# Optimization experiments

Measured on AMD Instinct MI355X. Metric: run time of the kernel, lower is better.

The kernel has to match this reference:

```python
import jax, jax.numpy as jnp
import numpy as np

N = 50000          # nodes
E = 800000         # directed edges (before self-loops)
IN_C = 512
HID = 256
HEADS = 8
HEAD_C = HID // HEADS
OUT_C = 64
NEG_SLOPE = 0.2    # PyG GATConv default LeakyReLU slope
EPS = 1e-16        # PyG softmax denominator epsilon


def _gat_layer(h, src, dst, a_src, a_dst):
    """One GATConv propagate step (eval mode, no attention dropout).
    h: [N, H, C] transformed node features; src/dst: [Etot] edge endpoints.
    Returns aggregated [N, H, C]."""
    # per-node attention logits: [N, H]
    alpha_src = jnp.einsum('nhc,hc->nh', h, a_src)
    alpha_dst = jnp.einsum('nhc,hc->nh', h, a_dst)
    e = alpha_src[src] + alpha_dst[dst]                      # [Etot, H]
    e = jnp.where(e > 0, e, NEG_SLOPE * e)                   # LeakyReLU
    # segment softmax over incoming edges of each dst node
    e_max = jax.ops.segment_max(e, dst, num_segments=N)      # [N, H]
    e_exp = jnp.exp(e - e_max[dst])                          # [Etot, H]
    denom = jax.ops.segment_sum(e_exp, dst, num_segments=N)  # [N, H]
    alpha = e_exp / (denom[dst] + EPS)                       # [Etot, H]
    msg = alpha[:, :, None] * h[src]                         # [Etot, H, C]
    return jax.ops.segment_sum(msg, dst, num_segments=N)     # [N, H, C]


def setup_inputs() -> dict:
    key = jax.random.key(0)
    ks = jax.random.split(key, 10)
    s1 = 1.0 / np.sqrt(IN_C)
    s2 = 1.0 / np.sqrt(HID)
    return {
        'x': jax.random.normal(ks[0], (N, IN_C), jnp.float32),
        'edge_index': jax.random.randint(ks[1], (2, E), 0, N, dtype=jnp.int64),
        'W1': jax.random.normal(ks[2], (IN_C, HID), jnp.float32) * s1,
        'a_src1': jax.random.normal(ks[3], (HEADS, HEAD_C), jnp.float32) * 0.1,
        'a_dst1': jax.random.normal(ks[4], (HEADS, HEAD_C), jnp.float32) * 0.1,
        'b1': jnp.zeros((HID,), jnp.float32),
        'W2': jax.random.normal(ks[5], (HID, OUT_C), jnp.float32) * s2,
        'a_src2': jax.random.normal(ks[6], (1, OUT_C), jnp.float32) * 0.1,
        'a_dst2': jax.random.normal(ks[7], (1, OUT_C), jnp.float32) * 0.1,
        'b2': jnp.zeros((OUT_C,), jnp.float32),
    }


def reference(x, edge_index, W1, a_src1, a_dst1, b1, W2, a_src2, a_dst2, b2):
    # PyG GATConv: add self-loops (default add_self_loops=True)
    loops = jnp.arange(N, dtype=edge_index.dtype)
    src = jnp.concatenate([edge_index[0], loops])
    dst = jnp.concatenate([edge_index[1], loops])

    # conv1: heads=8, concat=True
    h1 = (x @ W1).reshape(N, HEADS, HEAD_C)
    h1 = _gat_layer(h1, src, dst, a_src1, a_dst1).reshape(N, HID) + b1
    h1 = jax.nn.elu(h1)

    # conv2: heads=1, concat=False (mean over 1 head == identity)
    h2 = (h1 @ W2).reshape(N, 1, OUT_C)
    out = _gat_layer(h2, src, dst, a_src2, a_dst2).mean(axis=1) + b2
    return out
```

## Files before the change

### kernel.cpp

```cpp
#include <hip/hip_runtime.h>

#define N_NODES 50000
#define M_PAD   50048
#define NBLK    196
#define E_EDGES 800000
#define E_TOT   (E_EDGES + N_NODES)
#define IN_C 512
#define HID 256
#define HEADS 8
#define OUT_C 64

typedef unsigned int uint;
typedef unsigned short ushort_t;
typedef __bf16 bf16x8 __attribute__((ext_vector_type(8)));
typedef float f32x4 __attribute__((ext_vector_type(4)));
typedef float f32x2 __attribute__((ext_vector_type(2)));

__device__ __forceinline__ float lrelu(float x) { return x > 0.f ? x : 0.2f * x; }

__device__ __forceinline__ unsigned short f2bf(float f) {
  __bf16 b = (__bf16)f;
  return __builtin_bit_cast(unsigned short, b);
}
__device__ __forceinline__ float bflo(uint u) { return __uint_as_float(u << 16); }
__device__ __forceinline__ float bfhi(uint u) { return __uint_as_float(u & 0xFFFF0000u); }
__device__ __forceinline__ f32x2 unp2(uint u) {
  f32x2 r; r.x = bflo(u); r.y = bfhi(u); return r;
}

__global__ void k_count(const int* __restrict__ ei, int* __restrict__ counts) {
  int e = blockIdx.x * blockDim.x + threadIdx.x;
  if (e >= E_TOT) return;
  int d = (e < E_EDGES) ? ei[E_EDGES + e] : (e - E_EDGES);
  atomicAdd(&counts[d], 1);
}

__global__ void k_bsum(const int* __restrict__ counts, int* __restrict__ bsum) {
  int i = blockIdx.x * 256 + threadIdx.x;
  int v = (i < N_NODES) ? counts[i] : 0;
  __shared__ int ws[4];
  int lane = threadIdx.x & 63, wid = threadIdx.x >> 6;
  #pragma unroll
  for (int off = 32; off; off >>= 1) v += __shfl_xor(v, off);
  if (lane == 0) ws[wid] = v;
  __syncthreads();
  if (threadIdx.x == 0) bsum[blockIdx.x] = ws[0] + ws[1] + ws[2] + ws[3];
}

__global__ void k_bscan(const int* __restrict__ bsum, int* __restrict__ boff) {
  int tid = threadIdx.x;
  int v = (tid < NBLK) ? bsum[tid] : 0;
  int lane = tid & 63, wid = tid >> 6;
  int x = v;
  #pragma unroll
  for (int off = 1; off < 64; off <<= 1) {
    int t = __shfl_up(x, off);
    if (lane >= off) x += t;
  }
  __shared__ int ws[4];
  if (lane == 63) ws[wid] = x;
  __syncthreads();
  int woff = 0;
  for (int w = 0; w < wid; w++) woff += ws[w];
  if (tid < NBLK) boff[tid] = x + woff - v;
}

__global__ void k_local(const int* __restrict__ counts, const int* __restrict__ boff,
                        int* __restrict__ indptr, int* __restrict__ wptr) {
  int b = blockIdx.x;
  int i = b * 256 + threadIdx.x;
  int v = (i < N_NODES) ? counts[i] : 0;
  int lane = threadIdx.x & 63, wid = threadIdx.x >> 6;
  int x = v;
  #pragma unroll
  for (int off = 1; off < 64; off <<= 1) {
    int t = __shfl_up(x, off);
    if (lane >= off) x += t;
  }
  __shared__ int ws[4];
  if (lane == 63) ws[wid] = x;
  __syncthreads();
  int woff = boff[b];
  for (int w = 0; w < wid; w++) woff += ws[w];
  int excl = woff + x - v;
  if (i < N_NODES) { indptr[i] = excl; wptr[i] = excl; }
  if (b == 0 && threadIdx.x == 0) indptr[N_NODES] = E_TOT;
}

__global__ void k_scatter(const int* __restrict__ ei, int* __restrict__ wptr,
                          int* __restrict__ csr_src) {
  int e = blockIdx.x * blockDim.x + threadIdx.x;
  if (e >= E_TOT) return;
  int s, d;
  if (e < E_EDGES) { s = ei[e]; d = ei[E_EDGES + e]; }
  else { s = d = e - E_EDGES; }
  int pos = atomicAdd(&wptr[d], 1);
  csr_src[pos] = s;
}

__global__ void k_convw(const float* __restrict__ W1, const float* __restrict__ W2,
                        ushort_t* __restrict__ w1t, ushort_t* __restrict__ w2t) {
  int t = blockIdx.x * blockDim.x + threadIdx.x;
  if (t < HID * IN_C) {
    int n = t >> 9, k = t & 511;
    w1t[t] = f2bf(W1[(size_t)k * HID + n]);
  } else if (t < HID * IN_C + OUT_C * HID) {
    int u = t - HID * IN_C;
    int n = u >> 8, k = u & 255;
    w2t[u] = f2bf(W2[(size_t)k * OUT_C + n]);
  }
}

__global__ __launch_bounds__(512) void k_mm1(const float* __restrict__ A,
                                             const ushort_t* __restrict__ Bt,
                                             const float* __restrict__ asrc1,
                                             const float* __restrict__ adst1,
                                             ushort_t* __restrict__ Cb,
                                             float* __restrict__ as1,
                                             float* __restrict__ ad1) {
  __shared__ ushort_t sA[128][40];
  __shared__ ushort_t sB[256][40];
  int tid = threadIdx.x;
  int wid = tid >> 6, lane = tid & 63;
  int wm = wid >> 2, wn = wid & 3;
  int lr = lane & 15, kg = lane >> 4;
  int row0 = blockIdx.x * 128;
  f32x4 acc[4][4] = {};

  for (int k0 = 0; k0 < IN_C; k0 += 32) {
    {
      int r = tid >> 2, cs = (tid & 3) * 8;
      int gr = row0 + r;
      unsigned short v[8];
      if (gr < N_NODES) {
        const float* src = A + (size_t)gr * IN_C + k0 + cs;
        float4 f0 = *reinterpret_cast<const float4*>(src);
        float4 f1 = *reinterpret_cast<const float4*>(src + 4);
        v[0] = f2bf(f0.x); v[1] = f2bf(f0.y); v[2] = f2bf(f0.z); v[3] = f2bf(f0.w);
        v[4] = f2bf(f1.x); v[5] = f2bf(f1.y); v[6] = f2bf(f1.z); v[7] = f2bf(f1.w);
      } else {
        #pragma unroll
        for (int i = 0; i < 8; i++) v[i] = 0;
      }
      uint4 pk;
      pk.x = v[0] | ((uint)v[1] << 16); pk.y = v[2] | ((uint)v[3] << 16);
      pk.z = v[4] | ((uint)v[5] << 16); pk.w = v[6] | ((uint)v[7] << 16);
      *reinterpret_cast<uint4*>(&sA[r][cs]) = pk;
    }
    {
      int n = tid >> 1, ks = (tid & 1) * 16;
      const ushort_t* src = Bt + (size_t)n * IN_C + k0 + ks;
      uint4 v0 = *reinterpret_cast<const uint4*>(src);
      uint4 v1 = *reinterpret_cast<const uint4*>(src + 8);
      *reinterpret_cast<uint4*>(&sB[n][ks]) = v0;
      *reinterpret_cast<uint4*>(&sB[n][ks + 8]) = v1;
    }
    __syncthreads();

    bf16x8 af[4], bfr[4];
    #pragma unroll
    for (int i = 0; i < 4; i++)
      af[i] = *reinterpret_cast<const bf16x8*>(&sA[wm * 64 + i * 16 + lr][kg * 8]);
    #pragma unroll
    for (int j = 0; j < 4; j++)
      bfr[j] = *reinterpret_cast<const bf16x8*>(&sB[wn * 64 + j * 16 + lr][kg * 8]);
    #pragma unroll
    for (int i = 0; i < 4; i++)
      #pragma unroll
      for (int j = 0; j < 4; j++)
        acc[i][j] = __builtin_amdgcn_mfma_f32_16x16x32_bf16(af[i], bfr[j], acc[i][j], 0, 0, 0);
    __syncthreads();
  }

  {
    int h0 = wn * 2, h1 = wn * 2 + 1;
    float a0s = asrc1[h0 * 32 + lr], a1s = asrc1[h0 * 32 + 16 + lr];
    float a2s = asrc1[h1 * 32 + lr], a3s = asrc1[h1 * 32 + 16 + lr];
    float a0d = adst1[h0 * 32 + lr], a1d = adst1[h0 * 32 + 16 + lr];
    float a2d = adst1[h1 * 32 + lr], a3d = adst1[h1 * 32 + 16 + lr];
    #pragma unroll
    for (int i = 0; i < 4; i++) {
      #pragma unroll
      for (int q = 0; q < 4; q++) {
        float s0 = acc[i][0][q] * a0s + acc[i][1][q] * a1s;
        float s1 = acc[i][2][q] * a2s + acc[i][3][q] * a3s;
        float d0 = acc[i][0][q] * a0d + acc[i][1][q] * a1d;
        float d1 = acc[i][2][q] * a2d + acc[i][3][q] * a3d;
        #pragma unroll
        for (int off = 1; off < 16; off <<= 1) {
          s0 += __shfl_xor(s0, off);
          s1 += __shfl_xor(s1, off);
          d0 += __shfl_xor(d0, off);
          d1 += __shfl_xor(d1, off);
        }
        int gr = row0 + wm * 64 + i * 16 + kg * 4 + q;
        if (lr == 0 && gr < N_NODES) {
          as1[gr * 8 + h0] = s0;
          as1[gr * 8 + h1] = s1;
          ad1[gr * 8 + h0] = d0;
          ad1[gr * 8 + h1] = d1;
        }
      }
    }
  }

  #pragma unroll
  for (int i = 0; i < 4; i++) {
    #pragma unroll
    for (int j = 0; j < 4; j++) {
      int gc = wn * 64 + j * 16 + lr;
      #pragma unroll
      for (int q = 0; q < 4; q++) {
        int gr = row0 + wm * 64 + i * 16 + kg * 4 + q;
        if (gr < N_NODES) Cb[(size_t)gr * HID + gc] = f2bf(acc[i][j][q]);
      }
    }
  }
}

__global__ __launch_bounds__(256) void k_mm2(const ushort_t* __restrict__ At,
                                             const ushort_t* __restrict__ Bt,
                                             const float* __restrict__ asrc2,
                                             const float* __restrict__ adst2,
                                             ushort_t* __restrict__ Cb,
                                             float* __restrict__ as2,
                                             float* __restrict__ ad2) {
  __shared__ ushort_t sA[128][40];
  __shared__ ushort_t sB[64][40];
  int tid = threadIdx.x;
  int wid = tid >> 6, lane = tid & 63;
  int lr = lane & 15, kg = lane >> 4;
  int row0 = blockIdx.x * 128;
  f32x4 acc[2][4] = {};

  for (int kt = 0; kt < HID / 32; ++kt) {
    {
      const ushort_t* src = At + ((size_t)blockIdx.x * 8 + kt) * 4096 + tid * 16;
      uint4 v0 = *reinterpret_cast<const uint4*>(src);
      uint4 v1 = *reinterpret_cast<const uint4*>(src + 8);
      int r = tid >> 1, ks = (tid & 1) * 16;
      *reinterpret_cast<uint4*>(&sA[r][ks]) = v0;
      *reinterpret_cast<uint4*>(&sA[r][ks + 8]) = v1;
    }
    if (tid < 128) {
      int n = tid >> 1, ks = (tid & 1) * 16;
      const ushort_t* src = Bt + (size_t)n * HID + kt * 32 + ks;
      uint4 v0 = *reinterpret_cast<const uint4*>(src);
      uint4 v1 = *reinterpret_cast<const uint4*>(src + 8);
      *reinterpret_cast<uint4*>(&sB[n][ks]) = v0;
      *reinterpret_cast<uint4*>(&sB[n][ks + 8]) = v1;
    }
    __syncthreads();

    bf16x8 af[2], bfr[4];
    #pragma unroll
    for (int i = 0; i < 2; i++)
      af[i] = *reinterpret_cast<const bf16x8*>(&sA[wid * 32 + i * 16 + lr][kg * 8]);
    #pragma unroll
    for (int j = 0; j < 4; j++)
      bfr[j] = *reinterpret_cast<const bf16x8*>(&sB[j * 16 + lr][kg * 8]);
    #pragma unroll
    for (int i = 0; i < 2; i++)
      #pragma unroll
      for (int j = 0; j < 4; j++)
        acc[i][j] = __builtin_amdgcn_mfma_f32_16x16x32_bf16(af[i], bfr[j], acc[i][j], 0, 0, 0);
    __syncthreads();
  }

  {
    float avs[4], avd[4];
    #pragma unroll
    for (int j = 0; j < 4; j++) {
      avs[j] = asrc2[j * 16 + lr];
      avd[j] = adst2[j * 16 + lr];
    }
    #pragma unroll
    for (int i = 0; i < 2; i++) {
      #pragma unroll
      for (int q = 0; q < 4; q++) {
        float s = acc[i][0][q] * avs[0] + acc[i][1][q] * avs[1]
                + acc[i][2][q] * avs[2] + acc[i][3][q] * avs[3];
        float d = acc[i][0][q] * avd[0] + acc[i][1][q] * avd[1]
                + acc[i][2][q] * avd[2] + acc[i][3][q] * avd[3];
        #pragma unroll
        for (int off = 1; off < 16; off <<= 1) {
          s += __shfl_xor(s, off);
          d += __shfl_xor(d, off);
        }
        int gr = row0 + wid * 32 + i * 16 + kg * 4 + q;
        if (lr == 0 && gr < N_NODES) { as2[gr] = s; ad2[gr] = d; }
      }
    }
  }

  #pragma unroll
  for (int i = 0; i < 2; i++) {
    #pragma unroll
    for (int j = 0; j < 4; j++) {
      int gc = j * 16 + lr;
      #pragma unroll
      for (int q = 0; q < 4; q++) {
        int gr = row0 + wid * 32 + i * 16 + kg * 4 + q;
        if (gr < N_NODES) Cb[(size_t)gr * OUT_C + gc] = f2bf(acc[i][j][q]);
      }
    }
  }
}

__global__ __launch_bounds__(256) void k_agg1(const ushort_t* __restrict__ h1b,
                                              const int* __restrict__ indptr,
                                              const int* __restrict__ csr_src,
                                              const float* __restrict__ as1,
                                              const float* __restrict__ ad1,
                                              const float* __restrict__ b1,
                                              ushort_t* __restrict__ hpb) {
  int wave = threadIdx.x >> 6, lane = threadIdx.x & 63;
  int node = blockIdx.x * 4 + wave;
  if (node >= N_NODES) return;
  int beg = indptr[node], end = indptr[node + 1];
  int half = lane >> 5, sl = lane & 31, h = sl >> 2;
  float adst = ad1[node * 8 + h];

  f32x2 a0 = {0.f, 0.f}, a1 = {0.f, 0.f}, a2 = {0.f, 0.f}, a3 = {0.f, 0.f};
  float dsum = 0.f;
  int e = beg + half;
  for (; e + 6 < end; e += 8) {
    int s0 = csr_src[e];
    int s1 = csr_src[e + 2];
    int s2 = csr_src[e + 4];
    int s3 = csr_src[e + 6];
    float l0 = as1[s0 * 8 + h];
    float l1 = as1[s1 * 8 + h];
    float l2 = as1[s2 * 8 + h];
    float l3 = as1[s3 * 8 + h];
    uint4 r0 = *reinterpret_cast<const uint4*>(&h1b[(size_t)s0 * HID + sl * 8]);
    uint4 r1 = *reinterpret_cast<const uint4*>(&h1b[(size_t)s1 * HID + sl * 8]);
    uint4 r2 = *reinterpret_cast<const uint4*>(&h1b[(size_t)s2 * HID + sl * 8]);
    uint4 r3 = *reinterpret_cast<const uint4*>(&h1b[(size_t)s3 * HID + sl * 8]);
    float w0 = __expf(lrelu(l0 + adst));
    float w1 = __expf(lrelu(l1 + adst));
    float w2 = __expf(lrelu(l2 + adst));
    float w3 = __expf(lrelu(l3 + adst));
    a0 += w0 * unp2(r0.x); a1 += w0 * unp2(r0.y); a2 += w0 * unp2(r0.z); a3 += w0 * unp2(r0.w);
    a0 += w1 * unp2(r1.x); a1 += w1 * unp2(r1.y); a2 += w1 * unp2(r1.z); a3 += w1 * unp2(r1.w);
    a0 += w2 * unp2(r2.x); a1 += w2 * unp2(r2.y); a2 += w2 * unp2(r2.z); a3 += w2 * unp2(r2.w);
    a0 += w3 * unp2(r3.x); a1 += w3 * unp2(r3.y); a2 += w3 * unp2(r3.z); a3 += w3 * unp2(r3.w);
    dsum += w0 + w1 + w2 + w3;
  }
  for (; e < end; e += 2) {
    int s = csr_src[e];
    float w = __expf(lrelu(as1[s * 8 + h] + adst));
    uint4 rv = *reinterpret_cast<const uint4*>(&h1b[(size_t)s * HID + sl * 8]);
    a0 += w * unp2(rv.x); a1 += w * unp2(rv.y); a2 += w * unp2(rv.z); a3 += w * unp2(rv.w);
    dsum += w;
  }
  float acc[8] = {a0.x, a0.y, a1.x, a1.y, a2.x, a2.y, a3.x, a3.y};
  #pragma unroll
  for (int j = 0; j < 8; j++) acc[j] += __shfl_xor(acc[j], 32);
  dsum += __shfl_xor(dsum, 32);
  float inv = 1.f / (dsum + 1e-16f);

  if (half == 0) {
    unsigned short ob[8];
    #pragma unroll
    for (int j = 0; j < 8; j++) {
      float o = acc[j] * inv + b1[sl * 8 + j];
      o = o > 0.f ? o : expm1f(o);
      ob[j] = f2bf(o);
    }
    uint4 pk;
    pk.x = ob[0] | ((uint)ob[1] << 16); pk.y = ob[2] | ((uint)ob[3] << 16);
    pk.z = ob[4] | ((uint)ob[5] << 16); pk.w = ob[6] | ((uint)ob[7] << 16);
    size_t addr = ((size_t)(node >> 7) * 8 + (sl >> 2)) * 4096 + (size_t)(node & 127) * 32 + (sl & 3) * 8;
    *reinterpret_cast<uint4*>(&hpb[addr]) = pk;
  }
}

__global__ __launch_bounds__(256) void k_agg2(const ushort_t* __restrict__ h2b,
                                              const int* __restrict__ indptr,
                                              const int* __restrict__ csr_src,
                                              const float* __restrict__ as2,
                                              const float* __restrict__ ad2,
                                              const float* __restrict__ b2,
                                              float* __restrict__ out) {
  int wave = threadIdx.x >> 6, lane = threadIdx.x & 63;
  int node = blockIdx.x * 4 + wave;
  if (node >= N_NODES) return;
  int beg = indptr[node], end = indptr[node + 1];
  int half = lane >> 5, sl = lane & 31;
  float adst = ad2[node];

  f32x2 acc2 = {0.f, 0.f};
  float dsum = 0.f;
  int e = beg + half;
  for (; e + 6 < end; e += 8) {
    int s0 = csr_src[e];
    int s1 = csr_src[e + 2];
    int s2 = csr_src[e + 4];
    int s3 = csr_src[e + 6];
    float l0 = as2[s0];
    float l1 = as2[s1];
    float l2 = as2[s2];
    float l3 = as2[s3];
    uint v0 = *reinterpret_cast<const uint*>(&h2b[(size_t)s0 * OUT_C + sl * 2]);
    uint v1 = *reinterpret_cast<const uint*>(&h2b[(size_t)s1 * OUT_C + sl * 2]);
    uint v2 = *reinterpret_cast<const uint*>(&h2b[(size_t)s2 * OUT_C + sl * 2]);
    uint v3 = *reinterpret_cast<const uint*>(&h2b[(size_t)s3 * OUT_C + sl * 2]);
    float w0 = __expf(lrelu(l0 + adst));
    float w1 = __expf(lrelu(l1 + adst));
    float w2 = __expf(lrelu(l2 + adst));
    float w3 = __expf(lrelu(l3 + adst));
    acc2 += w0 * unp2(v0); acc2 += w1 * unp2(v1);
    acc2 += w2 * unp2(v2); acc2 += w3 * unp2(v3);
    dsum += w0 + w1 + w2 + w3;
  }
  for (; e < end; e += 2) {
    int s = csr_src[e];
    float w = __expf(lrelu(as2[s] + adst));
    uint v = *reinterpret_cast<const uint*>(&h2b[(size_t)s * OUT_C + sl * 2]);
    acc2 += w * unp2(v);
    dsum += w;
  }
  acc2.x += __shfl_xor(acc2.x, 32);
  acc2.y += __shfl_xor(acc2.y, 32);
  dsum += __shfl_xor(dsum, 32);
  float inv = 1.f / (dsum + 1e-16f);
  if (half == 0) {
    float2 o = {acc2.x * inv + b2[sl * 2], acc2.y * inv + b2[sl * 2 + 1]};
    *reinterpret_cast<float2*>(&out[(size_t)node * OUT_C + sl * 2]) = o;
  }
}

extern "C" void kernel_launch(void* const* d_in, const int* in_sizes, int n_in,
                              void* d_out, int out_size, void* d_ws, size_t ws_size,
                              hipStream_t stream) {
  const float* x     = (const float*)d_in[0];
  const int*   ei    = (const int*)d_in[1];
  const float* W1    = (const float*)d_in[2];
  const float* asrc1 = (const float*)d_in[3];
  const float* adst1 = (const float*)d_in[4];
  const float* b1    = (const float*)d_in[5];
  const float* W2    = (const float*)d_in[6];
  const float* asrc2 = (const float*)d_in[7];
  const float* adst2 = (const float*)d_in[8];
  const float* b2    = (const float*)d_in[9];
  float* out = (float*)d_out;

  char* p = (char*)d_ws;
  size_t off = 0;
  auto take = [&](size_t bytes) -> void* {
    void* r = p + off;
    off += (bytes + 255) & ~(size_t)255;
    return r;
  };
  ushort_t* h1b  = (ushort_t*)take((size_t)N_NODES * HID * 2);
  ushort_t* hpb  = (ushort_t*)take((size_t)(M_PAD / 128) * 8 * 4096 * 2);
  ushort_t* h2b  = (ushort_t*)take((size_t)N_NODES * OUT_C * 2);
  float*    as1  = (float*)take((size_t)N_NODES * HEADS * 4);
  float*    ad1  = (float*)take((size_t)N_NODES * HEADS * 4);
  float*    as2  = (float*)take((size_t)N_NODES * 4);
  float*    ad2  = (float*)take((size_t)N_NODES * 4);
  int* counts = (int*)take((size_t)N_NODES * 4);
  int* indptr = (int*)take((size_t)(N_NODES + 1) * 4);
  int* wptr   = (int*)take((size_t)(N_NODES + 1) * 4);
  int* bsum   = (int*)take((size_t)NBLK * 4);
  int* boff   = (int*)take((size_t)NBLK * 4);
  int* csr    = (int*)take((size_t)E_TOT * 4);
  ushort_t* w1t = (ushort_t*)take((size_t)IN_C * HID * 2);
  ushort_t* w2t = (ushort_t*)take((size_t)HID * OUT_C * 2);

  hipMemsetAsync(counts, 0, (size_t)N_NODES * 4, stream);
  k_count<<<(E_TOT + 255) / 256, 256, 0, stream>>>(ei, counts);
  k_bsum<<<NBLK, 256, 0, stream>>>(counts, bsum);
  k_bscan<<<1, 256, 0, stream>>>(bsum, boff);
  k_local<<<NBLK, 256, 0, stream>>>(counts, boff, indptr, wptr);
  k_scatter<<<(E_TOT + 255) / 256, 256, 0, stream>>>(ei, wptr, csr);

  k_convw<<<(HID * IN_C + OUT_C * HID + 255) / 256, 256, 0, stream>>>(W1, W2, w1t, w2t);

  k_mm1<<<M_PAD / 128, 512, 0, stream>>>(x, w1t, asrc1, adst1, h1b, as1, ad1);
  k_agg1<<<(N_NODES + 3) / 4, 256, 0, stream>>>(h1b, indptr, csr, as1, ad1, b1, hpb);

  k_mm2<<<M_PAD / 128, 256, 0, stream>>>(hpb, w2t, asrc2, adst2, h2b, as2, ad2);
  k_agg2<<<(N_NODES + 3) / 4, 256, 0, stream>>>(h2b, indptr, csr, as2, ad2, b2, out);
}
```

Before: 265.5 us.

## Fuse independent kernels into block-partitioned launches to overlap work

Merges the edge-count kernel with the weight transpose/convert kernel into one launch, and merges the CSR scatter with the first GEMM into another launch. Block index ranges select which job each block does, so the independent jobs run concurrently and there are two fewer launches. The GEMM only depends on the weight conversion and the scatter only on the prefix scan, so ordering stays correct. The cost is that the scatter's atomics now compete with the GEMM blocks for compute units, and the scatter blocks are scheduled after the GEMM blocks.

```diff
diff --git a/kernel.cpp b/kernel.cpp
--- a/kernel.cpp
+++ b/kernel.cpp
@@ -10,6 +10,12 @@
 #define HEADS 8
 #define OUT_C 64
 
+#define MM1_BLOCKS (M_PAD / 128)
+#define SCAT_BLOCKS ((E_TOT + 511) / 512)
+#define CNT_BLOCKS  ((E_TOT + 511) / 512)
+#define CONVW_ELEMS (HID * IN_C + OUT_C * HID)
+#define CONVW_BLOCKS ((CONVW_ELEMS + 511) / 512)
+
 typedef unsigned int uint;
 typedef unsigned short ushort_t;
 typedef __bf16 bf16x8 __attribute__((ext_vector_type(8)));
@@ -28,11 +34,29 @@
   f32x2 r; r.x = bflo(u); r.y = bfhi(u); return r;
 }
 
-__global__ void k_count(const int* __restrict__ ei, int* __restrict__ counts) {
-  int e = blockIdx.x * blockDim.x + threadIdx.x;
-  if (e >= E_TOT) return;
-  int d = (e < E_EDGES) ? ei[E_EDGES + e] : (e - E_EDGES);
-  atomicAdd(&counts[d], 1);
+__global__ __launch_bounds__(512) void k_fatA(const int* __restrict__ ei,
+                                              int* __restrict__ counts,
+                                              const float* __restrict__ W1,
+                                              const float* __restrict__ W2,
+                                              ushort_t* __restrict__ w1t,
+                                              ushort_t* __restrict__ w2t) {
+  int bid = blockIdx.x;
+  if (bid < CNT_BLOCKS) {
+    int e = bid * 512 + threadIdx.x;
+    if (e >= E_TOT) return;
+    int d = (e < E_EDGES) ? ei[E_EDGES + e] : (e - E_EDGES);
+    atomicAdd(&counts[d], 1);
+  } else {
+    int t = (bid - CNT_BLOCKS) * 512 + threadIdx.x;
+    if (t < HID * IN_C) {
+      int n = t >> 9, k = t & 511;
+      w1t[t] = f2bf(W1[(size_t)k * HID + n]);
+    } else if (t < CONVW_ELEMS) {
+      int u = t - HID * IN_C;
+      int n = u >> 8, k = u & 255;
+      w2t[u] = f2bf(W2[(size_t)k * OUT_C + n]);
+    }
+  }
 }
 
 __global__ void k_bsum(const int* __restrict__ counts, int* __restrict__ bsum) {
@@ -87,37 +111,26 @@
   if (b == 0 && threadIdx.x == 0) indptr[N_NODES] = E_TOT;
 }
 
-__global__ void k_scatter(const int* __restrict__ ei, int* __restrict__ wptr,
-                          int* __restrict__ csr_src) {
-  int e = blockIdx.x * blockDim.x + threadIdx.x;
-  if (e >= E_TOT) return;
-  int s, d;
-  if (e < E_EDGES) { s = ei[e]; d = ei[E_EDGES + e]; }
-  else { s = d = e - E_EDGES; }
-  int pos = atomicAdd(&wptr[d], 1);
-  csr_src[pos] = s;
-}
-
-__global__ void k_convw(const float* __restrict__ W1, const float* __restrict__ W2,
-                        ushort_t* __restrict__ w1t, ushort_t* __restrict__ w2t) {
-  int t = blockIdx.x * blockDim.x + threadIdx.x;
-  if (t < HID * IN_C) {
-    int n = t >> 9, k = t & 511;
-    w1t[t] = f2bf(W1[(size_t)k * HID + n]);
-  } else if (t < HID * IN_C + OUT_C * HID) {
-    int u = t - HID * IN_C;
-    int n = u >> 8, k = u & 255;
-    w2t[u] = f2bf(W2[(size_t)k * OUT_C + n]);
-  }
-}
-
-__global__ __launch_bounds__(512) void k_mm1(const float* __restrict__ A,
-                                             const ushort_t* __restrict__ Bt,
-                                             const float* __restrict__ asrc1,
-                                             const float* __restrict__ adst1,
-                                             ushort_t* __restrict__ Cb,
-                                             float* __restrict__ as1,
-                                             float* __restrict__ ad1) {
+__global__ __launch_bounds__(512) void k_fatB(const float* __restrict__ A,
+                                              const ushort_t* __restrict__ Bt,
+                                              const float* __restrict__ asrc1,
+                                              const float* __restrict__ adst1,
+                                              ushort_t* __restrict__ Cb,
+                                              float* __restrict__ as1,
+                                              float* __restrict__ ad1,
+                                              const int* __restrict__ ei,
+                                              int* __restrict__ wptr,
+                                              int* __restrict__ csr_src) {
+  if (blockIdx.x >= MM1_BLOCKS) {
+    int e = (blockIdx.x - MM1_BLOCKS) * 512 + threadIdx.x;
+    if (e >= E_TOT) return;
+    int s, d;
+    if (e < E_EDGES) { s = ei[e]; d = ei[E_EDGES + e]; }
+    else { s = d = e - E_EDGES; }
+    int pos = atomicAdd(&wptr[d], 1);
+    csr_src[pos] = s;
+    return;
+  }
   __shared__ ushort_t sA[128][40];
   __shared__ ushort_t sB[256][40];
   int tid = threadIdx.x;
@@ -470,15 +483,14 @@
   ushort_t* w2t = (ushort_t*)take((size_t)HID * OUT_C * 2);
 
   hipMemsetAsync(counts, 0, (size_t)N_NODES * 4, stream);
-  k_count<<<(E_TOT + 255) / 256, 256, 0, stream>>>(ei, counts);
+  k_fatA<<<CNT_BLOCKS + CONVW_BLOCKS, 512, 0, stream>>>(ei, counts, W1, W2, w1t, w2t);
   k_bsum<<<NBLK, 256, 0, stream>>>(counts, bsum);
   k_bscan<<<1, 256, 0, stream>>>(bsum, boff);
   k_local<<<NBLK, 256, 0, stream>>>(counts, boff, indptr, wptr);
-  k_scatter<<<(E_TOT + 255) / 256, 256, 0, stream>>>(ei, wptr, csr);
-
-  k_convw<<<(HID * IN_C + OUT_C * HID + 255) / 256, 256, 0, stream>>>(W1, W2, w1t, w2t);
-
-  k_mm1<<<M_PAD / 128, 512, 0, stream>>>(x, w1t, asrc1, adst1, h1b, as1, ad1);
+
+  k_fatB<<<MM1_BLOCKS + SCAT_BLOCKS, 512, 0, stream>>>(x, w1t, asrc1, adst1, h1b, as1, ad1,
+                                                       ei, wptr, csr);
+
   k_agg1<<<(N_NODES + 3) / 4, 256, 0, stream>>>(h1b, indptr, csr, as1, ad1, b1, hpb);
 
   k_mm2<<<M_PAD / 128, 256, 0, stream>>>(hpb, w2t, asrc2, adst2, h2b, as2, ad2);
```

After: 240.8 us. 9.3% less time.
